# Optimization experiments

Measured on AMD Instinct MI355X. Metric: run time of the kernel, lower is better.

The kernel has to match this reference:

```python
import jax, jax.numpy as jnp
import numpy as np

T = 0.09   # softmax temperature
M = 0.7    # momentum for key-encoder update
DIM, K, B, L, P = 128, 65536, 1024, 512, 8388608

def _l2norm(x, axis):
    return x / jnp.linalg.norm(x, axis=axis, keepdims=True)

def setup_inputs() -> dict:
    key = jax.random.key(0)
    ks = jax.random.split(key, 6)
    q = jax.random.normal(ks[0], (B, DIM), jnp.float32)
    queue = _l2norm(jax.random.normal(ks[1], (DIM, K), jnp.float32), axis=0)  # columns normalized as in __init__
    keys = jax.random.normal(ks[2], (B, DIM), jnp.float32)
    param_q = jax.random.normal(ks[3], (P,), jnp.float32)
    param_k = jax.random.normal(ks[4], (P,), jnp.float32)
    sample_idx = jax.random.randint(ks[5], (B, L), 0, K, jnp.int32)  # col 0 = positive sample index
    return {"q": q, "queue": queue, "keys": keys, "param_q": param_q,
            "param_k": param_k, "sample_idx": sample_idx, "ptr": 0}

def reference(q, queue, keys, param_q, param_k, sample_idx, ptr):
    # q = F.normalize(q, dim=1)
    qn = _l2norm(q, axis=1)
    # per-sample ragged gather of queue columns, batched: queue[:, idx] for each sample list
    cols = jnp.take(queue.T, sample_idx, axis=0)            # [B, L, DIM]
    # logits = einsum('c,ck->k', q_i, gathered_i), stacked + padded, / T
    logits = jnp.einsum('bld,bd->bl', cols, qn) / T         # [B, L]
    labels = jnp.zeros((B,), jnp.int32)                     # positive is index 0
    # momentum update of key-encoder params: k = m*k + (1-m)*q
    new_param_k = param_k * M + param_q * (1.0 - M)
    # dequeue/enqueue: queue[:, ptr:ptr+B] = normalize(keys).T (circular write)
    new_queue = jax.lax.dynamic_update_slice(queue, _l2norm(keys, axis=1).T, (0, ptr))
    return (logits, labels, new_queue, new_param_k)
```

## Files before the change

### kernel.cpp

```cpp
#include <hip/hip_runtime.h>
#include <stdint.h>

#define DIM   128
#define KCOLS 65536
#define BB    1024
#define LL    512
#define PSZ   8388608
#define INV_T (1.0f / 0.09f)
#define MOM   0.7f

#define OUT_LOGITS 0
#define OUT_LABELS (BB * LL)
#define OUT_QUEUE  (BB * LL + BB)
#define OUT_PARAMK (BB * LL + BB + DIM * KCOLS)

#define WS_QT 0
#define WS_QN (KCOLS * DIM * 2)
#define WS_KN (WS_QN + BB * DIM * 4)

__device__ inline unsigned short f32_to_bf16(float f) {
    uint32_t u = __float_as_uint(f);
    uint32_t r = (u + 0x7fffu + ((u >> 16) & 1u)) >> 16;
    return (unsigned short)r;
}

__global__ void norm_kernel(const float* __restrict__ q,
                            const float* __restrict__ keys,
                            float* __restrict__ qn, float* __restrict__ kn) {
    int w    = threadIdx.x >> 6;
    int lane = threadIdx.x & 63;
    int row  = blockIdx.x * 4 + w;
    const float* src;
    float* dst;
    int r;
    if (row < BB) { src = q;    dst = qn; r = row; }
    else          { src = keys; dst = kn; r = row - BB; }
    float2 v = *(const float2*)&src[r * DIM + lane * 2];
    float s  = v.x * v.x + v.y * v.y;
#pragma unroll
    for (int m = 32; m >= 1; m >>= 1) s += __shfl_xor(s, m, 64);
    float inv = 1.0f / sqrtf(s);
    float2 o  = {v.x * inv, v.y * inv};
    *(float2*)&dst[r * DIM + lane * 2] = o;
}

__global__ void param_kernel(const float* __restrict__ pq,
                             const float* __restrict__ pk,
                             float* __restrict__ out) {
    int gid  = blockIdx.x * blockDim.x + threadIdx.x;
    float4 a = ((const float4*)pq)[gid];
    float4 b = ((const float4*)pk)[gid];
    float4 r;
    r.x = b.x * MOM + a.x * (1.0f - MOM);
    r.y = b.y * MOM + a.y * (1.0f - MOM);
    r.z = b.z * MOM + a.z * (1.0f - MOM);
    r.w = b.w * MOM + a.w * (1.0f - MOM);
    ((float4*)(out + OUT_PARAMK))[gid] = r;
    if (gid < BB) out[OUT_LABELS + gid] = 0.0f;
}

__global__ void queue_fused_kernel(const float* __restrict__ queue,
                                   const float* __restrict__ kn,
                                   const int* __restrict__ ptr_p,
                                   float* __restrict__ outq,
                                   unsigned short* __restrict__ qt) {
    __shared__ float tile[64][DIM + 1];
    int k0 = blockIdx.x * 64;
    int t  = threadIdx.x;
    int kk = t & 63, dq = t >> 6;
    int ptr   = ptr_p[0];
    int start = min(max(ptr, 0), KCOLS - BB);
    int k     = k0 + kk;
    bool inwin = (k >= start) && (k < start + BB);
#pragma unroll
    for (int i = 0; i < 32; ++i) {
        int d = i * 4 + dq;
        float v = queue[d * KCOLS + k];
        tile[kk][d] = v;
        float w = inwin ? kn[(k - start) * DIM + d] : v;
        outq[d * KCOLS + k] = w;
    }
    __syncthreads();
    int lane16 = t & 15, kq = t >> 4;
#pragma unroll
    for (int ki = 0; ki < 4; ++ki) {
        int kl = kq + ki * 16;
#pragma unroll
        for (int seg = 0; seg < 4; ++seg) {
            int d0 = seg * 32 + lane16 * 2;
            uint32_t lo = (uint32_t)f32_to_bf16(tile[kl][d0]);
            uint32_t hi = (uint32_t)f32_to_bf16(tile[kl][d0 + 1]);
            *(uint32_t*)&qt[(size_t)(k0 + kl) * DIM + d0] = lo | (hi << 16);
        }
    }
}

__global__ void logits_kernel(const float* __restrict__ qn,
                              const unsigned short* __restrict__ qt,
                              const int* __restrict__ sidx,
                              float* __restrict__ out_logits) {
    int b    = blockIdx.y;
    int t    = threadIdx.x;
    int wave = t >> 6;
    int lane = t & 63;
    int quarter = lane & 3;
    int lg      = lane >> 2;

    float qreg[32];
    const float4* qb = (const float4*)(qn + b * DIM + quarter * 32);
#pragma unroll
    for (int i = 0; i < 8; ++i) {
        float4 v = qb[i];
        qreg[4 * i + 0] = v.x; qreg[4 * i + 1] = v.y;
        qreg[4 * i + 2] = v.z; qreg[4 * i + 3] = v.w;
    }

    int l = blockIdx.x * 64 + wave * 16 + lg;
    int idx = sidx[b * LL + l];
    const uint4* p = (const uint4*)(qt + (size_t)idx * DIM + quarter * 32);
    float s0 = 0.f, s1 = 0.f, s2 = 0.f, s3 = 0.f;
#pragma unroll
    for (int c = 0; c < 4; ++c) {
        uint4 u = p[c];
        float acc = 0.f;
        acc += qreg[c * 8 + 0] * __uint_as_float(u.x << 16);
        acc += qreg[c * 8 + 1] * __uint_as_float(u.x & 0xffff0000u);
        acc += qreg[c * 8 + 2] * __uint_as_float(u.y << 16);
        acc += qreg[c * 8 + 3] * __uint_as_float(u.y & 0xffff0000u);
        acc += qreg[c * 8 + 4] * __uint_as_float(u.z << 16);
        acc += qreg[c * 8 + 5] * __uint_as_float(u.z & 0xffff0000u);
        acc += qreg[c * 8 + 6] * __uint_as_float(u.w << 16);
        acc += qreg[c * 8 + 7] * __uint_as_float(u.w & 0xffff0000u);
        if (c == 0) s0 = acc; else if (c == 1) s1 = acc;
        else if (c == 2) s2 = acc; else s3 = acc;
    }
    float s = (s0 + s1) + (s2 + s3);
    s += __shfl_xor(s, 1, 64);
    s += __shfl_xor(s, 2, 64);
    if (quarter == 0) out_logits[b * LL + l] = s * INV_T;
}

extern "C" void kernel_launch(void* const* d_in, const int* in_sizes, int n_in,
                              void* d_out, int out_size, void* d_ws, size_t ws_size,
                              hipStream_t stream) {
    const float* q     = (const float*)d_in[0];
    const float* queue = (const float*)d_in[1];
    const float* keys  = (const float*)d_in[2];
    const float* pq    = (const float*)d_in[3];
    const float* pk    = (const float*)d_in[4];
    const int*   sidx  = (const int*)d_in[5];
    const int*   ptr_p = (const int*)d_in[6];
    float* out = (float*)d_out;

    unsigned short* ws_qt = (unsigned short*)((char*)d_ws + WS_QT);
    float* ws_qn = (float*)((char*)d_ws + WS_QN);
    float* ws_kn = (float*)((char*)d_ws + WS_KN);

    norm_kernel<<<512, 256, 0, stream>>>(q, keys, ws_qn, ws_kn);
    queue_fused_kernel<<<KCOLS / 64, 256, 0, stream>>>(queue, ws_kn, ptr_p,
                                                       out + OUT_QUEUE, ws_qt);
    param_kernel<<<PSZ / 4 / 256, 256, 0, stream>>>(pq, pk, out);
    logits_kernel<<<dim3(LL / 64, BB), 256, 0, stream>>>(ws_qn, ws_qt, sidx,
                                                         out + OUT_LOGITS);
}
```

Measured before the change: 213.5 us.

## Bin logits gathers by XCD-local queue slice and vectorize queue transpose

The logits kernel now uses a 1D grid of B*8 blocks. Each block filters its sample row to the indices whose queue column falls in a 8192-column slice matching blockIdx&7, on the assumption that round-robin dispatch places each block on a fixed XCD so that XCD's L2 holds only a 1/8 slice of the bf16 transposed queue. The queue transpose kernel also switches to float4 loads and stores and uint4 bf16 packing. The binning adds an LDS atomic compaction pass, reads sample_idx twice, and gives blocks uneven work.

```diff
diff --git a/kernel.cpp b/kernel.cpp
--- a/kernel.cpp
+++ b/kernel.cpp
@@ -67,44 +67,70 @@
     __shared__ float tile[64][DIM + 1];
     int k0 = blockIdx.x * 64;
     int t  = threadIdx.x;
-    int kk = t & 63, dq = t >> 6;
     int ptr   = ptr_p[0];
     int start = min(max(ptr, 0), KCOLS - BB);
-    int k     = k0 + kk;
-    bool inwin = (k >= start) && (k < start + BB);
+
+    int lane16 = t & 15;
+    int hi     = t >> 4;
+    int kq     = lane16 * 4;
 #pragma unroll
-    for (int i = 0; i < 32; ++i) {
-        int d = i * 4 + dq;
-        float v = queue[d * KCOLS + k];
-        tile[kk][d] = v;
-        float w = inwin ? kn[(k - start) * DIM + d] : v;
-        outq[d * KCOLS + k] = w;
+    for (int p = 0; p < 8; ++p) {
+        int d = p * 16 + hi;
+        float4 v = *(const float4*)&queue[(size_t)d * KCOLS + k0 + kq];
+        float vv[4] = {v.x, v.y, v.z, v.w};
+#pragma unroll
+        for (int j = 0; j < 4; ++j) {
+            tile[kq + j][d] = vv[j];
+            int col = k0 + kq + j;
+            if (col >= start && col < start + BB)
+                vv[j] = kn[(size_t)(col - start) * DIM + d];
+        }
+        float4 w = {vv[0], vv[1], vv[2], vv[3]};
+        *(float4*)&outq[(size_t)d * KCOLS + k0 + kq] = w;
     }
     __syncthreads();
-    int lane16 = t & 15, kq = t >> 4;
+    int d0 = lane16 * 8;
 #pragma unroll
     for (int ki = 0; ki < 4; ++ki) {
-        int kl = kq + ki * 16;
+        int kl = hi + ki * 16;
+        float f[8];
 #pragma unroll
-        for (int seg = 0; seg < 4; ++seg) {
-            int d0 = seg * 32 + lane16 * 2;
-            uint32_t lo = (uint32_t)f32_to_bf16(tile[kl][d0]);
-            uint32_t hi = (uint32_t)f32_to_bf16(tile[kl][d0 + 1]);
-            *(uint32_t*)&qt[(size_t)(k0 + kl) * DIM + d0] = lo | (hi << 16);
-        }
+        for (int j = 0; j < 8; ++j) f[j] = tile[kl][d0 + j];
+        uint4 o;
+        o.x = (uint32_t)f32_to_bf16(f[0]) | ((uint32_t)f32_to_bf16(f[1]) << 16);
+        o.y = (uint32_t)f32_to_bf16(f[2]) | ((uint32_t)f32_to_bf16(f[3]) << 16);
+        o.z = (uint32_t)f32_to_bf16(f[4]) | ((uint32_t)f32_to_bf16(f[5]) << 16);
+        o.w = (uint32_t)f32_to_bf16(f[6]) | ((uint32_t)f32_to_bf16(f[7]) << 16);
+        *(uint4*)&qt[(size_t)(k0 + kl) * DIM + d0] = o;
     }
 }
 
-__global__ void logits_kernel(const float* __restrict__ qn,
-                              const unsigned short* __restrict__ qt,
-                              const int* __restrict__ sidx,
-                              float* __restrict__ out_logits) {
-    int b    = blockIdx.y;
-    int t    = threadIdx.x;
-    int wave = t >> 6;
-    int lane = t & 63;
-    int quarter = lane & 3;
-    int lg      = lane >> 2;
+__global__ void __launch_bounds__(256)
+logits_kernel(const float* __restrict__ qn,
+              const unsigned short* __restrict__ qt,
+              const int* __restrict__ sidx,
+              float* __restrict__ out_logits) {
+    int b   = blockIdx.x >> 3;
+    int xcd = blockIdx.x & 7;
+    int t   = threadIdx.x;
+
+    __shared__ unsigned short lst[LL];
+    __shared__ int n;
+    if (t == 0) n = 0;
+    __syncthreads();
+#pragma unroll
+    for (int l = t; l < LL; l += 256) {
+        int idx = sidx[b * LL + l];
+        if ((idx >> 13) == xcd) {
+            int p = atomicAdd(&n, 1);
+            lst[p] = (unsigned short)l;
+        }
+    }
+    __syncthreads();
+    int cnt = n;
+
+    int quarter = t & 3;
+    int grp     = t >> 2;
 
     float qreg[32];
     const float4* qb = (const float4*)(qn + b * DIM + quarter * 32);
@@ -115,29 +141,31 @@
         qreg[4 * i + 2] = v.z; qreg[4 * i + 3] = v.w;
     }
 
-    int l = blockIdx.x * 64 + wave * 16 + lg;
-    int idx = sidx[b * LL + l];
-    const uint4* p = (const uint4*)(qt + (size_t)idx * DIM + quarter * 32);
-    float s0 = 0.f, s1 = 0.f, s2 = 0.f, s3 = 0.f;
+    for (int i = grp; i < cnt; i += 64) {
+        int l   = lst[i];
+        int idx = sidx[b * LL + l];
+        const uint4* p = (const uint4*)(qt + (size_t)idx * DIM + quarter * 32);
+        float s0 = 0.f, s1 = 0.f, s2 = 0.f, s3 = 0.f;
 #pragma unroll
-    for (int c = 0; c < 4; ++c) {
-        uint4 u = p[c];
-        float acc = 0.f;
-        acc += qreg[c * 8 + 0] * __uint_as_float(u.x << 16);
-        acc += qreg[c * 8 + 1] * __uint_as_float(u.x & 0xffff0000u);
-        acc += qreg[c * 8 + 2] * __uint_as_float(u.y << 16);
-        acc += qreg[c * 8 + 3] * __uint_as_float(u.y & 0xffff0000u);
-        acc += qreg[c * 8 + 4] * __uint_as_float(u.z << 16);
-        acc += qreg[c * 8 + 5] * __uint_as_float(u.z & 0xffff0000u);
-        acc += qreg[c * 8 + 6] * __uint_as_float(u.w << 16);
-        acc += qreg[c * 8 + 7] * __uint_as_float(u.w & 0xffff0000u);
-        if (c == 0) s0 = acc; else if (c == 1) s1 = acc;
-        else if (c == 2) s2 = acc; else s3 = acc;
+        for (int c = 0; c < 4; ++c) {
+            uint4 u = p[c];
+            float acc = 0.f;
+            acc += qreg[c * 8 + 0] * __uint_as_float(u.x << 16);
+            acc += qreg[c * 8 + 1] * __uint_as_float(u.x & 0xffff0000u);
+            acc += qreg[c * 8 + 2] * __uint_as_float(u.y << 16);
+            acc += qreg[c * 8 + 3] * __uint_as_float(u.y & 0xffff0000u);
+            acc += qreg[c * 8 + 4] * __uint_as_float(u.z << 16);
+            acc += qreg[c * 8 + 5] * __uint_as_float(u.z & 0xffff0000u);
+            acc += qreg[c * 8 + 6] * __uint_as_float(u.w << 16);
+            acc += qreg[c * 8 + 7] * __uint_as_float(u.w & 0xffff0000u);
+            if (c == 0) s0 = acc; else if (c == 1) s1 = acc;
+            else if (c == 2) s2 = acc; else s3 = acc;
+        }
+        float s = (s0 + s1) + (s2 + s3);
+        s += __shfl_xor(s, 1, 64);
+        s += __shfl_xor(s, 2, 64);
+        if (quarter == 0) out_logits[b * LL + l] = s * INV_T;
     }
-    float s = (s0 + s1) + (s2 + s3);
-    s += __shfl_xor(s, 1, 64);
-    s += __shfl_xor(s, 2, 64);
-    if (quarter == 0) out_logits[b * LL + l] = s * INV_T;
 }
 
 extern "C" void kernel_launch(void* const* d_in, const int* in_sizes, int n_in,
@@ -160,6 +188,6 @@
     queue_fused_kernel<<<KCOLS / 64, 256, 0, stream>>>(queue, ws_kn, ptr_p,
                                                        out + OUT_QUEUE, ws_qt);
     param_kernel<<<PSZ / 4 / 256, 256, 0, stream>>>(pq, pk, out);
-    logits_kernel<<<dim3(LL / 64, BB), 256, 0, stream>>>(ws_qn, ws_qt, sidx,
-                                                         out + OUT_LOGITS);
+    logits_kernel<<<BB * 8, 256, 0, stream>>>(ws_qn, ws_qt, sidx,
+                                              out + OUT_LOGITS);
 }
```

After: 213.1 us. Within noise of the previous version (-0.2%).
